# Kernel optimization log

Hardware: AMD Instinct MI355X
Metric: run time of the kernel (lower is better)

The kernel has to match this reference:

```python
import jax, jax.numpy as jnp
import numpy as np

N_E, N_U, N_D = 512, 256, 256
N_A = 16
N_FB = 4
N_SV = 256
N_PV = 64
D_IN0 = 3 * (4 * N_A) + 2 * 4   # 200, fb_block output at layer 0
D_IN = 3 * N_SV + 2 * N_PV      # 896, fb_block output thereafter


def _fb_block(s_v, p_v):
    # s_v: (n_e, d_s); p_v: (n_e, n_e, d_p)
    n_e = N_U + N_D
    su_m = jnp.tile(s_v[:N_U].mean(0)[None, :], (n_e, 1))
    sd_m = jnp.tile(s_v[N_U:].mean(0)[None, :], (n_e, 1))
    pu_m = p_v[:N_U].mean(0)   # (n_e, d_p)
    pd_m = p_v[N_U:].mean(0)
    return jnp.concatenate([su_m, sd_m, pu_m, pd_m, s_v], axis=-1)


def setup_inputs() -> dict:
    key = jax.random.key(0)
    ks = jax.random.split(key, 16)

    def lin(k, fin, fout):
        k1, k2 = jax.random.split(k)
        lim = 1.0 / np.sqrt(fin)
        W = jax.random.uniform(k1, (fin, fout), minval=-lim, maxval=lim, dtype=jnp.float32)
        b = jax.random.uniform(k2, (fout,), minval=-lim, maxval=lim, dtype=jnp.float32)
        return W, b

    V0_W, V0_b = lin(ks[0], D_IN0, N_SV)
    W0_W, W0_b = lin(ks[1], 4, N_PV)
    VrW, Vrb, WrW, Wrb = [], [], [], []
    for i in range(N_FB - 1):
        w, b = lin(ks[2 + i], D_IN, N_SV); VrW.append(w); Vrb.append(b)
        w, b = lin(ks[6 + i], N_PV, N_PV); WrW.append(w); Wrb.append(b)
    Vr_W, Vr_b = jnp.stack(VrW), jnp.stack(Vrb)
    Wr_W, Wr_b = jnp.stack(WrW), jnp.stack(Wrb)
    Vhu_W, Vhu_b = lin(ks[10], D_IN, N_SV)
    Vhd_W, Vhd_b = lin(ks[11], D_IN, N_SV)
    wu_W, wu_b = lin(ks[12], N_SV, N_U)
    wd_W, wd_b = lin(ks[13], N_SV, N_D)
    r = jax.random.normal(ks[14], (N_E, 3), dtype=jnp.float32)
    a = jax.random.normal(ks[15], (N_A, 3), dtype=jnp.float32) * 2.0
    return dict(r=r, a=a, V0_W=V0_W, V0_b=V0_b, Vr_W=Vr_W, Vr_b=Vr_b,
                W0_W=W0_W, W0_b=W0_b, Wr_W=Wr_W, Wr_b=Wr_b,
                Vhu_W=Vhu_W, Vhu_b=Vhu_b, Vhd_W=Vhd_W, Vhd_b=Vhd_b,
                wu_W=wu_W, wu_b=wu_b, wd_W=wd_W, wd_b=wd_b)


def reference(r, a, V0_W, V0_b, Vr_W, Vr_b, W0_W, W0_b, Wr_W, Wr_b,
              Vhu_W, Vhu_b, Vhd_W, Vhd_b, wu_W, wu_b, wd_W, wd_b):
    n_e = N_E
    eye = jnp.eye(n_e, dtype=r.dtype)[:, :, None]
    ra = r[:, None, :] - a[None, :, :]                       # (n_e, n_a, 3)
    ra_len = jnp.linalg.norm(ra, axis=-1, keepdims=True)
    rr = r[None, :, :] - r[:, None, :]                       # (n_e, n_e, 3)
    rr_len = jnp.linalg.norm(rr + eye, axis=-1, keepdims=True)
    s_v = jnp.concatenate([ra, ra_len], axis=-1).reshape(n_e, -1)   # (n_e, 4*n_a)
    p_v = jnp.concatenate([rr, rr_len], axis=-1)                    # (n_e, n_e, 4)
    s_blk = _fb_block(s_v, p_v)
    for l in range(N_FB):
        VW, Vb = (V0_W, V0_b) if l == 0 else (Vr_W[l - 1], Vr_b[l - 1])
        WW, Wb = (W0_W, W0_b) if l == 0 else (Wr_W[l - 1], Wr_b[l - 1])
        s_new = jnp.tanh(s_blk @ VW + Vb)
        s_v = s_new + s_v if s_v.shape[-1] == N_SV else s_new   # residual skips layer 0
        p_new = jnp.tanh(p_v @ WW + Wb)
        p_v = p_new + p_v if p_v.shape[-1] == N_PV else p_new
        s_blk = _fb_block(s_v, p_v)
    s_u = jnp.tanh(s_blk[:N_U] @ Vhu_W + Vhu_b)
    s_d = jnp.tanh(s_blk[N_U:] @ Vhd_W + Vhd_b)
    s_wu = s_u @ wu_W + wu_b                                  # (n_u, n_u)
    s_wd = s_d @ wd_W + wd_b                                  # (n_d, n_d)
    exp_u = jnp.linalg.norm(ra[:N_U], axis=-1, keepdims=True)  # (n_u, n_a, 1)
    exp_d = jnp.linalg.norm(ra[N_U:], axis=-1, keepdims=True)
    orb_u = (s_wu * jnp.exp(-exp_u).sum(axis=1))[None]         # (1, n_u, n_u)
    orb_d = (s_wd * jnp.exp(-exp_d).sum(axis=1))[None]
    # logabssumdet with n_det == 1, matrix dim > 1
    sgn_u, log_u = jnp.linalg.slogdet(orb_u)
    sgn_d, log_d = jnp.linalg.slogdet(orb_d)
    psi = (sgn_u * sgn_d * jnp.exp(log_u + log_d)).sum()
    return jnp.log(jnp.abs(psi))
```

## Files before the change

### kernel.cpp

```cpp
#include <hip/hip_runtime.h>
#include <hip/hip_bf16.h>

#define NE 512

__device__ __align__(16) float g_sv0[NE*64];
__device__ __align__(16) float g_sv[2][NE*256];
__device__ __align__(16) float g_pu4[NE*4];
__device__ __align__(16) float g_pd4[NE*4];
__device__ __align__(16) float g_puL[4*NE*64];
__device__ __align__(16) float g_pdL[4*NE*64];
__device__ __align__(16) float g_su0[64];
__device__ __align__(16) float g_sd0[64];
__device__ __align__(16) float g_su[256];
__device__ __align__(16) float g_sd[256];
__device__ __align__(16) float g_part4[4*16*NE*64];
__device__ __align__(16) float g_f[NE];
__device__ __align__(16) float g_hu[256*256];
__device__ __align__(16) float g_hd[256*256];
__device__ __align__(16) float g_orbu[256*256];
__device__ __align__(16) float g_orbd[256*256];
__device__ float g_logs[2];

__device__ __forceinline__ float tanh_fast(float x) {
  float e = __expf(2.f * x);
  return 1.f - 2.f / (e + 1.f);
}

__global__ __launch_bounds__(256) void k_pgeom(const float* __restrict__ r,
                                               const float* __restrict__ a) {
  int j = blockIdx.x, t = threadIdx.x;
  if (j == 0) {
    for (int h = 0; h < 2; ++h) {
      int e = h*256 + t;
      float rx = r[3*e], ry = r[3*e+1], rz = r[3*e+2];
      float facc = 0.f;
      #pragma unroll
      for (int at = 0; at < 16; ++at) {
        float dx = rx - a[3*at], dy = ry - a[3*at+1], dz = rz - a[3*at+2];
        float len = sqrtf(dx*dx + dy*dy + dz*dz);
        g_sv0[e*64 + 4*at + 0] = dx;
        g_sv0[e*64 + 4*at + 1] = dy;
        g_sv0[e*64 + 4*at + 2] = dz;
        g_sv0[e*64 + 4*at + 3] = len;
        facc += expf(-len);
      }
      g_f[e] = facc;
    }
    __syncthreads();
    if (t < 128) {
      int h = t >> 6, c = t & 63;
      float s = 0.f;
      for (int i = 0; i < 256; ++i) s += g_sv0[(h*256 + i)*64 + c];
      (h ? g_sd0 : g_su0)[c] = s * (1.f/256.f);
    }
    __syncthreads();
  }
  float rjx = r[3*j], rjy = r[3*j+1], rjz = r[3*j+2];
  __shared__ float red[4][4];
  for (int h = 0; h < 2; ++h) {
    int i = h*256 + t;
    float dx = rjx - r[3*i], dy = rjy - r[3*i+1], dz = rjz - r[3*i+2];
    float ee = (i == j) ? 1.f : 0.f;
    float ex = dx+ee, ey = dy+ee, ez = dz+ee;
    float len = sqrtf(ex*ex + ey*ey + ez*ez);
    float v0 = dx, v1 = dy, v2 = dz, v3 = len;
    #pragma unroll
    for (int m = 1; m < 64; m <<= 1) {
      v0 += __shfl_xor(v0, m); v1 += __shfl_xor(v1, m);
      v2 += __shfl_xor(v2, m); v3 += __shfl_xor(v3, m);
    }
    if ((t & 63) == 0) {
      int wv = t >> 6;
      red[wv][0]=v0; red[wv][1]=v1; red[wv][2]=v2; red[wv][3]=v3;
    }
    __syncthreads();
    if (t == 0) {
      float* dst = h ? g_pd4 : g_pu4;
      #pragma unroll
      for (int c = 0; c < 4; ++c)
        dst[j*4 + c] = (red[0][c]+red[1][c]+red[2][c]+red[3][c]) * (1.f/256.f);
    }
    __syncthreads();
  }
}

__global__ __launch_bounds__(256, 4) void k_pchain(const float* __restrict__ W0,
                                                   const float* __restrict__ b0,
                                                   const float* __restrict__ Wr,
                                                   const float* __restrict__ brs,
                                                   const float* __restrict__ r) {
  __shared__ __align__(16) float xbuf[4][32*64];
  int t = threadIdx.x, lane = t & 63, wv = t >> 6;
  int gw = blockIdx.x*4 + wv;
  int j = gw >> 4, chunk = gw & 15;
  int i0 = chunk * 32;
  float* xb = xbuf[wv];
  float rjx = r[3*j], rjy = r[3*j+1], rjz = r[3*j+2];
  float macc0 = 0.f, macc1 = 0.f, macc2 = 0.f, macc3 = 0.f;
  {
    float w0 = W0[lane], w1 = W0[64+lane], w2 = W0[128+lane], w3 = W0[192+lane];
    float bb = b0[lane];
    for (int ii = 0; ii < 32; ++ii) {
      int i = i0 + ii;
      float dx = rjx - r[3*i], dy = rjy - r[3*i+1], dz = rjz - r[3*i+2];
      float ee = (i == j) ? 1.f : 0.f;
      float ex = dx+ee, ey = dy+ee, ez = dz+ee;
      float len = sqrtf(ex*ex + ey*ey + ez*ez);
      float y = tanh_fast(bb + dx*w0 + dy*w1 + dz*w2 + len*w3);
      xb[ii*64 + lane] = y;
      macc0 += y;
    }
  }
  for (int l = 0; l < 3; ++l) {
    const float* W = Wr + l*4096;
    float wcol[64];
    #pragma unroll
    for (int k = 0; k < 64; ++k) wcol[k] = W[k*64 + lane];
    float bb = brs[l*64 + lane];
    float mac = 0.f;
    for (int ii = 0; ii < 32; ++ii) {
      const float* row = &xb[ii*64];
      float x = row[lane];
      float acc = bb;
      #pragma unroll
      for (int g = 0; g < 16; ++g) {
        float4 pv = *(const float4*)&row[4*g];
        acc += pv.x*wcol[4*g] + pv.y*wcol[4*g+1] + pv.z*wcol[4*g+2] + pv.w*wcol[4*g+3];
      }
      float y = tanh_fast(acc) + x;
      xb[ii*64 + lane] = y;
      mac += y;
    }
    if (l == 0) macc1 = mac;
    else if (l == 1) macc2 = mac;
    else macc3 = mac;
  }
  int base = chunk*(NE*64) + j*64 + lane;
  g_part4[0*(16*NE*64) + base] = macc0;
  g_part4[1*(16*NE*64) + base] = macc1;
  g_part4[2*(16*NE*64) + base] = macc2;
  g_part4[3*(16*NE*64) + base] = macc3;
}

__global__ __launch_bounds__(256) void k_reduce_p() {
  int idx = blockIdx.x*256 + threadIdx.x;
  int l = idx >> 16;
  int rem = idx & 65535;
  int half = rem >> 15;
  int r2 = rem & 32767;
  int j = r2 >> 6, c = r2 & 63;
  const float* pp = g_part4 + l*(16*NE*64) + half*(8*NE*64) + j*64 + c;
  float s = 0.f;
  #pragma unroll
  for (int ch = 0; ch < 8; ++ch) s += pp[ch*(NE*64)];
  (half ? g_pdL : g_puL)[l*(NE*64) + j*64 + c] = s * (1.f/256.f);
}

__global__ __launch_bounds__(256) void k_smean(int svsel) {
  int h = blockIdx.x, t = threadIdx.x;
  const float* sv = g_sv[svsel];
  float s = 0.f;
  for (int i = 0; i < 256; ++i) s += sv[(h*256 + i)*256 + t];
  (h ? g_sd : g_su)[t] = s * (1.f/256.f);
}

template<int PUK, int SVK, int MEANK>
__global__ __launch_bounds__(256) void k_smm(int which, const float* __restrict__ W,
                                             const float* __restrict__ Wb,
                                             const float* __restrict__ W2,
                                             const float* __restrict__ Wb2,
                                             int pl) {
  constexpr int MAINK = 2*PUK + SVK;
  __shared__ __align__(16) float wsl[MAINK*32];
  __shared__ float insl[32*(MAINK+1)];
  __shared__ float biasv[32];
  __shared__ float bred[256];
  const float *pu_p=nullptr, *pd_p=nullptr, *sv_p=nullptr, *su_p=nullptr, *sd_p=nullptr;
  const float *res_p=nullptr, *rs_p=nullptr;
  float* out_p = nullptr;
  int t = threadIdx.x;
  int rg = blockIdx.x, cg = blockIdx.y;
  int grp = 0, rgl = rg;
  if (which >= 4) { grp = rg >> 3; rgl = rg & 7; }
  const float* Wsel = (which >= 4 && grp) ? W2 : W;
  const float* Wbsel = (which >= 4 && grp) ? Wb2 : Wb;
  int in_base = 0, dotanh = 1;
  switch (which) {
    case 0: pu_p=g_pu4; pd_p=g_pd4; su_p=g_su0; sd_p=g_sd0; sv_p=g_sv0;
            out_p=g_sv[0]; in_base=rg*32; break;
    case 1: case 2: case 3:
      pu_p=g_puL + pl*(NE*64); pd_p=g_pdL + pl*(NE*64); su_p=g_su; sd_p=g_sd;
      sv_p=g_sv[(which+1)&1]; res_p=sv_p; out_p=g_sv[which&1]; in_base=rg*32; break;
    case 4: pu_p=g_puL + pl*(NE*64); pd_p=g_pdL + pl*(NE*64); su_p=g_su; sd_p=g_sd;
            sv_p=g_sv[1]; out_p = grp ? g_hd : g_hu; in_base = grp*256 + rgl*32; break;
    default: sv_p = grp ? g_hd : g_hu; out_p = grp ? g_orbd : g_orbu;
             rs_p = g_f + grp*256; in_base = rgl*32; dotanh = 0; break;
  }
  int out_base = (which >= 4) ? rgl*32 : rg*32;
  int col0 = cg * 32;
  for (int idx = t; idx < MAINK*32; idx += 256) {
    int c = idx >> 5, cl = idx & 31;
    wsl[idx] = Wsel[(2*MEANK + c)*256 + col0 + cl];
  }
  for (int rr = 0; rr < 32; ++rr) {
    int row = in_base + rr;
    for (int c = t; c < MAINK; c += 256) {
      float v;
      if (c < PUK) v = pu_p[row*PUK + c];
      else if (c < 2*PUK) v = pd_p[row*PUK + (c - PUK)];
      else v = sv_p[row*SVK + (c - 2*PUK)];
      insl[rr*(MAINK+1) + c] = v;
    }
  }
  {
    int pcol = t & 31, ps = t >> 5;
    float bacc = 0.f;
    if (MEANK > 0) {
      for (int c = ps; c < MEANK; c += 8)
        bacc += su_p[c]*Wsel[c*256 + col0 + pcol] + sd_p[c]*Wsel[(MEANK + c)*256 + col0 + pcol];
    }
    bred[ps*32 + pcol] = bacc;
  }
  __syncthreads();
  if (t < 32) {
    float s = Wbsel[col0 + t];
    #pragma unroll
    for (int p8 = 0; p8 < 8; ++p8) s += bred[p8*32 + t];
    biasv[t] = s;
  }
  __syncthreads();
  int c4 = t & 7, rl = t >> 3;
  float a0 = biasv[4*c4], a1 = biasv[4*c4+1], a2 = biasv[4*c4+2], a3 = biasv[4*c4+3];
  const float* inrow = &insl[rl*(MAINK+1)];
  #pragma unroll 4
  for (int c = 0; c < MAINK; ++c) {
    float iv = inrow[c];
    float4 wv = *(const float4*)&wsl[c*32 + 4*c4];
    a0 += iv*wv.x; a1 += iv*wv.y; a2 += iv*wv.z; a3 += iv*wv.w;
  }
  int rowA = out_base + rl;
  int col = col0 + 4*c4;
  if (dotanh) { a0=tanh_fast(a0); a1=tanh_fast(a1); a2=tanh_fast(a2); a3=tanh_fast(a3); }
  if (res_p) {
    float4 rv = *(const float4*)&res_p[rowA*256 + col];
    a0 += rv.x; a1 += rv.y; a2 += rv.z; a3 += rv.w;
  }
  if (rs_p) { float fsc = rs_p[rowA]; a0*=fsc; a1*=fsc; a2*=fsc; a3*=fsc; }
  float4 ov; ov.x=a0; ov.y=a1; ov.z=a2; ov.w=a3;
  *(float4*)&out_p[rowA*256 + col] = ov;
}

#define REP8(M) M(0) M(1) M(2) M(3) M(4) M(5) M(6) M(7)
#define DPPMAX(v, CTRL) { unsigned _o = (unsigned)__builtin_amdgcn_update_dpp(0, (int)(v), CTRL, 0xf, 0xf, true); \
                          (v) = (v) > _o ? (v) : _o; }

__global__ __launch_bounds__(512, 2) void k_lu() {
  __shared__ __align__(16) float colbuf[2][256];
  __shared__ __align__(16) float prowbuf[2][16*20];
  const float* A = (blockIdx.x == 0) ? g_orbu : g_orbd;
  int t = threadIdx.x;
  int tile_c = t >> 5;
  int tile_r = t & 31;
  int lane = t & 63;
  int br = tile_r * 8;
  int pb = tile_c * 20;
  const float4* Ap = (const float4*)(A + br*256 + tile_c*16);
#define DECLROW(R) float4 M##R##_0 = Ap[R*64+0], M##R##_1 = Ap[R*64+1], \
                          M##R##_2 = Ap[R*64+2], M##R##_3 = Ap[R*64+3];
  REP8(DECLROW)
#undef DECLROW
  unsigned um = 0;
  if (tile_c == 0) {
#define INIT0(R) colbuf[0][br+R] = M##R##_0.x;
    REP8(INIT0)
#undef INIT0
  }
  __syncthreads();
  float prod = 1.f;
  int esum = 0;
  float m0=0,m1=0,m2=0,m3=0,m4=0,m5=0,m6=0,m7=0;
  for (int k = 0; k < 256; ++k) {
    const float* cbin = colbuf[k & 1];
    float4 cv = *(const float4*)&cbin[4*lane];
    float4 ca = *(const float4*)&cbin[br];
    float4 cb2 = *(const float4*)&cbin[br+4];
    bool aliveU = (tile_c*16 + 15) >= k;
    if (k > 0 && aliveU) {
      const float* pwp = &prowbuf[(k-1) & 1][pb];
      float4 P0 = *(const float4*)&pwp[0];
      float4 P1 = *(const float4*)&pwp[4];
      float4 P2 = *(const float4*)&pwp[8];
      float4 P3 = *(const float4*)&pwp[12];
#define UPD(R) { float mr = m##R; \
  M##R##_0.x -= mr*P0.x; M##R##_0.y -= mr*P0.y; M##R##_0.z -= mr*P0.z; M##R##_0.w -= mr*P0.w; \
  M##R##_1.x -= mr*P1.x; M##R##_1.y -= mr*P1.y; M##R##_1.z -= mr*P1.z; M##R##_1.w -= mr*P1.w; \
  M##R##_2.x -= mr*P2.x; M##R##_2.y -= mr*P2.y; M##R##_2.z -= mr*P2.z; M##R##_2.w -= mr*P2.w; \
  M##R##_3.x -= mr*P3.x; M##R##_3.y -= mr*P3.y; M##R##_3.z -= mr*P3.z; M##R##_3.w -= mr*P3.w; }
      REP8(UPD)
#undef UPD
    }
    unsigned b0 = (um & 1u) ? 0u : ((__float_as_uint(fabsf(cv.x)) & 0xFFFFFF00u) | (unsigned)(4*lane+0));
    unsigned b1 = (um & 2u) ? 0u : ((__float_as_uint(fabsf(cv.y)) & 0xFFFFFF00u) | (unsigned)(4*lane+1));
    unsigned b2 = (um & 4u) ? 0u : ((__float_as_uint(fabsf(cv.z)) & 0xFFFFFF00u) | (unsigned)(4*lane+2));
    unsigned b3 = (um & 8u) ? 0u : ((__float_as_uint(fabsf(cv.w)) & 0xFFFFFF00u) | (unsigned)(4*lane+3));
    unsigned bb = max(max(b0,b1), max(b2,b3));
    DPPMAX(bb, 0x111) DPPMAX(bb, 0x112) DPPMAX(bb, 0x114) DPPMAX(bb, 0x118)
    DPPMAX(bb, 0x142) DPPMAX(bb, 0x143)
    bb = (unsigned)__builtin_amdgcn_readlane((int)bb, 63);
    int p = (int)(bb & 255u);
    int wl = p >> 2, cc = p & 3;
    unsigned px = (unsigned)__builtin_amdgcn_readlane((int)__float_as_uint(cv.x), wl);
    unsigned py = (unsigned)__builtin_amdgcn_readlane((int)__float_as_uint(cv.y), wl);
    unsigned pz = (unsigned)__builtin_amdgcn_readlane((int)__float_as_uint(cv.z), wl);
    unsigned pw = (unsigned)__builtin_amdgcn_readlane((int)__float_as_uint(cv.w), wl);
    float piv = __uint_as_float(cc==0 ? px : cc==1 ? py : cc==2 ? pz : pw);
    int ee; float mant = frexpf(fabsf(piv), &ee);
    prod *= mant; esum += ee;
    if ((k & 31) == 31) { int e2; prod = frexpf(prod, &e2); esum += e2; }
    if (wl == lane) um |= 1u << cc;
    if (k == 255) break;
    float rp = 1.0f / piv;
    m0 = ca.x*rp; m1 = ca.y*rp; m2 = ca.z*rp; m3 = ca.w*rp;
    m4 = cb2.x*rp; m5 = cb2.y*rp; m6 = cb2.z*rp; m7 = cb2.w*rp;
    bool aliveK = (tile_c*16 + 15) > k;
    if (aliveK && tile_r == (p >> 3)) {
      float* pw_ = &prowbuf[k & 1][pb];
      switch (p & 7) {
#define PUBC(R) case R: *(float4*)&pw_[0] = M##R##_0; *(float4*)&pw_[4] = M##R##_1; \
                        *(float4*)&pw_[8] = M##R##_2; *(float4*)&pw_[12] = M##R##_3; break;
        REP8(PUBC)
#undef PUBC
      }
    }
    int kn = k + 1;
    if (tile_c == (kn >> 4)) {
      float e0,e1,e2b,e3,e4,e5,e6,e7;
      switch (kn & 15) {
#define EXTC(I, G, C) case I: e0=M0_##G.C; e1=M1_##G.C; e2b=M2_##G.C; e3=M3_##G.C; \
                              e4=M4_##G.C; e5=M5_##G.C; e6=M6_##G.C; e7=M7_##G.C; break;
        EXTC(0,0,x) EXTC(1,0,y) EXTC(2,0,z) EXTC(3,0,w)
        EXTC(4,1,x) EXTC(5,1,y) EXTC(6,1,z) EXTC(7,1,w)
        EXTC(8,2,x) EXTC(9,2,y) EXTC(10,2,z) EXTC(11,2,w)
        EXTC(12,3,x) EXTC(13,3,y) EXTC(14,3,z) EXTC(15,3,w)
#undef EXTC
      }
      float sel;
      switch (p & 7) {
        case 0: sel = e0; break; case 1: sel = e1; break;
        case 2: sel = e2b; break; case 3: sel = e3; break;
        case 4: sel = e4; break; case 5: sel = e5; break;
        case 6: sel = e6; break; default: sel = e7; break;
      }
      int srcl = __builtin_amdgcn_readfirstlane((tile_c & 1)*32 + (p >> 3));
      float pv = __uint_as_float((unsigned)__builtin_amdgcn_readlane(
                   (int)__float_as_uint(sel), srcl));
      float4 w0, w1;
      w0.x = e0 - m0*pv; w0.y = e1 - m1*pv; w0.z = e2b - m2*pv; w0.w = e3 - m3*pv;
      w1.x = e4 - m4*pv; w1.y = e5 - m5*pv; w1.z = e6 - m6*pv; w1.w = e7 - m7*pv;
      *(float4*)&colbuf[kn & 1][br] = w0;
      *(float4*)&colbuf[kn & 1][br+4] = w1;
    }
    __syncthreads();
  }
  if (t == 0) g_logs[blockIdx.x] = logf(prod) + (float)esum * 0.69314718055994531f;
}

__global__ void k_final(float* out) { out[0] = g_logs[0] + g_logs[1]; }

extern "C" void kernel_launch(void* const* d_in, const int* in_sizes, int n_in,
                              void* d_out, int out_size, void* d_ws, size_t ws_size,
                              hipStream_t stream) {
  const float* r     = (const float*)d_in[0];
  const float* a     = (const float*)d_in[1];
  const float* V0_W  = (const float*)d_in[2];
  const float* V0_b  = (const float*)d_in[3];
  const float* Vr_W  = (const float*)d_in[4];
  const float* Vr_b  = (const float*)d_in[5];
  const float* W0_W  = (const float*)d_in[6];
  const float* W0_b  = (const float*)d_in[7];
  const float* Wr_W  = (const float*)d_in[8];
  const float* Wr_b  = (const float*)d_in[9];
  const float* Vhu_W = (const float*)d_in[10];
  const float* Vhu_b = (const float*)d_in[11];
  const float* Vhd_W = (const float*)d_in[12];
  const float* Vhd_b = (const float*)d_in[13];
  const float* wu_W  = (const float*)d_in[14];
  const float* wu_b  = (const float*)d_in[15];
  const float* wd_W  = (const float*)d_in[16];
  const float* wd_b  = (const float*)d_in[17];
  float* out = (float*)d_out;

  k_pgeom<<<512, 256, 0, stream>>>(r, a);
  k_pchain<<<2048, 256, 0, stream>>>(W0_W, W0_b, Wr_W, Wr_b, r);
  k_reduce_p<<<1024, 256, 0, stream>>>();

  k_smm<4,64,64><<<dim3(16,8), 256, 0, stream>>>(0, V0_W, V0_b, nullptr, nullptr, 0);
  k_smean<<<2, 256, 0, stream>>>(0);
  k_smm<64,256,256><<<dim3(16,8), 256, 0, stream>>>(1, Vr_W + 0*896*256, Vr_b + 0,
                                                    nullptr, nullptr, 0);
  k_smean<<<2, 256, 0, stream>>>(1);
  k_smm<64,256,256><<<dim3(16,8), 256, 0, stream>>>(2, Vr_W + 1*896*256, Vr_b + 256,
                                                    nullptr, nullptr, 1);
  k_smean<<<2, 256, 0, stream>>>(0);
  k_smm<64,256,256><<<dim3(16,8), 256, 0, stream>>>(3, Vr_W + 2*896*256, Vr_b + 512,
                                                    nullptr, nullptr, 2);
  k_smean<<<2, 256, 0, stream>>>(1);
  k_smm<64,256,256><<<dim3(16,8), 256, 0, stream>>>(4, Vhu_W, Vhu_b, Vhd_W, Vhd_b, 3);
  k_smm<0,256,0><<<dim3(16,8), 256, 0, stream>>>(6, wu_W, wu_b, wd_W, wd_b, 0);
  k_lu<<<2, 512, 0, stream>>>();
  k_final<<<1, 1, 0, stream>>>(out);
}
```

Measured before the change: 650.9 us.

## Pipeline LU pivot search and defer trailing update off the critical path

The blocked LU kernel now computes the pivot search for the next column inside the wave that owns that column, reducing over only 32 rows with DPP, and publishes the pivot index and value through shared scalars. The full rank-1 update of each thread's register tile is deferred by one step: the pivot row and the next column get the previous update applied on the fly, and the bulk update runs after they are published. This is meant to shorten the serial dependency chain per iteration, since every wave no longer redoes a 256-wide argmax reduction and readlane sequence. In exchange the code carries extra per-iteration register state, and pivot selection moves to a partial reduction that needs the 32-row-per-wave layout to stay correct.

```diff
diff --git a/kernel.cpp b/kernel.cpp
--- a/kernel.cpp
+++ b/kernel.cpp
@@ -251,12 +251,12 @@
 }
 
 #define REP8(M) M(0) M(1) M(2) M(3) M(4) M(5) M(6) M(7)
-#define DPPMAX(v, CTRL) { unsigned _o = (unsigned)__builtin_amdgcn_update_dpp(0, (int)(v), CTRL, 0xf, 0xf, true); \
-                          (v) = (v) > _o ? (v) : _o; }
 
 __global__ __launch_bounds__(512, 2) void k_lu() {
   __shared__ __align__(16) float colbuf[2][256];
   __shared__ __align__(16) float prowbuf[2][16*20];
+  __shared__ unsigned scal_p[2];
+  __shared__ float scal_v[2];
   const float* A = (blockIdx.x == 0) ? g_orbu : g_orbd;
   int t = threadIdx.x;
   int tile_c = t >> 5;
@@ -269,99 +269,117 @@
                           M##R##_2 = Ap[R*64+2], M##R##_3 = Ap[R*64+3];
   REP8(DECLROW)
 #undef DECLROW
-  unsigned um = 0;
+  unsigned um8 = 0;
+#define DPAIR(CTRL) { unsigned ko = (unsigned)__builtin_amdgcn_update_dpp(0, (int)key, CTRL, 0xf, 0xf, true); \
+                      unsigned vo = (unsigned)__builtin_amdgcn_update_dpp(0, (int)__float_as_uint(val), CTRL, 0xf, 0xf, true); \
+                      if (ko > key) { key = ko; val = __uint_as_float(vo); } }
+#define CAND(RR) { unsigned kk = (um8 & (1u<<RR)) ? 0u : ((__float_as_uint(fabsf(e##RR)) & 0xFFFFFF00u) | (unsigned)(br + RR)); \
+                   if (kk > key) { key = kk; val = e##RR; } }
   if (tile_c == 0) {
-#define INIT0(R) colbuf[0][br+R] = M##R##_0.x;
-    REP8(INIT0)
-#undef INIT0
+    float e0 = M0_0.x, e1 = M1_0.x, e2 = M2_0.x, e3 = M3_0.x;
+    float e4 = M4_0.x, e5 = M5_0.x, e6 = M6_0.x, e7 = M7_0.x;
+    float4 w0; w0.x=e0; w0.y=e1; w0.z=e2; w0.w=e3;
+    float4 w1; w1.x=e4; w1.y=e5; w1.z=e6; w1.w=e7;
+    *(float4*)&colbuf[0][br] = w0;
+    *(float4*)&colbuf[0][br+4] = w1;
+    unsigned key = 0; float val = 0.f;
+    REP8(CAND)
+    DPAIR(0x111) DPAIR(0x112) DPAIR(0x114) DPAIR(0x118) DPAIR(0x142)
+    if (tile_r == 31) { scal_p[0] = key & 255u; scal_v[0] = val; }
   }
   __syncthreads();
   float prod = 1.f;
   int esum = 0;
-  float m0=0,m1=0,m2=0,m3=0,m4=0,m5=0,m6=0,m7=0;
+  float mp0=0,mp1=0,mp2=0,mp3=0,mp4=0,mp5=0,mp6=0,mp7=0;
   for (int k = 0; k < 256; ++k) {
-    const float* cbin = colbuf[k & 1];
-    float4 cv = *(const float4*)&cbin[4*lane];
-    float4 ca = *(const float4*)&cbin[br];
-    float4 cb2 = *(const float4*)&cbin[br+4];
-    bool aliveU = (tile_c*16 + 15) >= k;
-    if (k > 0 && aliveU) {
-      const float* pwp = &prowbuf[(k-1) & 1][pb];
-      float4 P0 = *(const float4*)&pwp[0];
-      float4 P1 = *(const float4*)&pwp[4];
-      float4 P2 = *(const float4*)&pwp[8];
-      float4 P3 = *(const float4*)&pwp[12];
-#define UPD(R) { float mr = m##R; \
-  M##R##_0.x -= mr*P0.x; M##R##_0.y -= mr*P0.y; M##R##_0.z -= mr*P0.z; M##R##_0.w -= mr*P0.w; \
-  M##R##_1.x -= mr*P1.x; M##R##_1.y -= mr*P1.y; M##R##_1.z -= mr*P1.z; M##R##_1.w -= mr*P1.w; \
-  M##R##_2.x -= mr*P2.x; M##R##_2.y -= mr*P2.y; M##R##_2.z -= mr*P2.z; M##R##_2.w -= mr*P2.w; \
-  M##R##_3.x -= mr*P3.x; M##R##_3.y -= mr*P3.y; M##R##_3.z -= mr*P3.z; M##R##_3.w -= mr*P3.w; }
-      REP8(UPD)
-#undef UPD
-    }
-    unsigned b0 = (um & 1u) ? 0u : ((__float_as_uint(fabsf(cv.x)) & 0xFFFFFF00u) | (unsigned)(4*lane+0));
-    unsigned b1 = (um & 2u) ? 0u : ((__float_as_uint(fabsf(cv.y)) & 0xFFFFFF00u) | (unsigned)(4*lane+1));
-    unsigned b2 = (um & 4u) ? 0u : ((__float_as_uint(fabsf(cv.z)) & 0xFFFFFF00u) | (unsigned)(4*lane+2));
-    unsigned b3 = (um & 8u) ? 0u : ((__float_as_uint(fabsf(cv.w)) & 0xFFFFFF00u) | (unsigned)(4*lane+3));
-    unsigned bb = max(max(b0,b1), max(b2,b3));
-    DPPMAX(bb, 0x111) DPPMAX(bb, 0x112) DPPMAX(bb, 0x114) DPPMAX(bb, 0x118)
-    DPPMAX(bb, 0x142) DPPMAX(bb, 0x143)
-    bb = (unsigned)__builtin_amdgcn_readlane((int)bb, 63);
-    int p = (int)(bb & 255u);
-    int wl = p >> 2, cc = p & 3;
-    unsigned px = (unsigned)__builtin_amdgcn_readlane((int)__float_as_uint(cv.x), wl);
-    unsigned py = (unsigned)__builtin_amdgcn_readlane((int)__float_as_uint(cv.y), wl);
-    unsigned pz = (unsigned)__builtin_amdgcn_readlane((int)__float_as_uint(cv.z), wl);
-    unsigned pw = (unsigned)__builtin_amdgcn_readlane((int)__float_as_uint(cv.w), wl);
-    float piv = __uint_as_float(cc==0 ? px : cc==1 ? py : cc==2 ? pz : pw);
+    int buf = k & 1;
+    unsigned pk = scal_p[buf];
+    float piv = scal_v[buf];
     int ee; float mant = frexpf(fabsf(piv), &ee);
     prod *= mant; esum += ee;
-    if ((k & 31) == 31) { int e2; prod = frexpf(prod, &e2); esum += e2; }
-    if (wl == lane) um |= 1u << cc;
+    if ((k & 31) == 31) { int e2n; prod = frexpf(prod, &e2n); esum += e2n; }
+    if ((int)(pk >> 3) == tile_r) um8 |= 1u << (pk & 7);
     if (k == 255) break;
     float rp = 1.0f / piv;
-    m0 = ca.x*rp; m1 = ca.y*rp; m2 = ca.z*rp; m3 = ca.w*rp;
-    m4 = cb2.x*rp; m5 = cb2.y*rp; m6 = cb2.z*rp; m7 = cb2.w*rp;
-    bool aliveK = (tile_c*16 + 15) > k;
-    if (aliveK && tile_r == (p >> 3)) {
-      float* pw_ = &prowbuf[k & 1][pb];
-      switch (p & 7) {
-#define PUBC(R) case R: *(float4*)&pw_[0] = M##R##_0; *(float4*)&pw_[4] = M##R##_1; \
-                        *(float4*)&pw_[8] = M##R##_2; *(float4*)&pw_[12] = M##R##_3; break;
-        REP8(PUBC)
-#undef PUBC
+    float4 c0 = *(const float4*)&colbuf[buf][br];
+    float4 c1 = *(const float4*)&colbuf[buf][br+4];
+    float m0 = c0.x*rp, m1 = c0.y*rp, m2 = c0.z*rp, m3 = c0.w*rp;
+    float m4 = c1.x*rp, m5 = c1.y*rp, m6 = c1.z*rp, m7 = c1.w*rp;
+    bool alive = (tile_c*16 + 15) >= (k + 1);
+    float4 PR0, PR1, PR2, PR3;
+    PR0.x=PR0.y=PR0.z=PR0.w=0.f; PR1=PR0; PR2=PR0; PR3=PR0;
+    bool havePR = (k > 0) && alive;
+    if (havePR) {
+      const float* pwp = &prowbuf[buf^1][pb];
+      PR0 = *(const float4*)&pwp[0];
+      PR1 = *(const float4*)&pwp[4];
+      PR2 = *(const float4*)&pwp[8];
+      PR3 = *(const float4*)&pwp[12];
+    }
+    float4 P0, P1, P2, P3;
+    P0.x=P0.y=P0.z=P0.w=0.f; P1=P0; P2=P0; P3=P0;
+    if (alive && (int)(pk >> 3) == tile_r) {
+      float mpsel = 0.f;
+      switch (pk & 7) {
+#define PSELR(R) case R: P0=M##R##_0; P1=M##R##_1; P2=M##R##_2; P3=M##R##_3; mpsel=mp##R; break;
+        REP8(PSELR)
+#undef PSELR
       }
+      P0.x -= mpsel*PR0.x; P0.y -= mpsel*PR0.y; P0.z -= mpsel*PR0.z; P0.w -= mpsel*PR0.w;
+      P1.x -= mpsel*PR1.x; P1.y -= mpsel*PR1.y; P1.z -= mpsel*PR1.z; P1.w -= mpsel*PR1.w;
+      P2.x -= mpsel*PR2.x; P2.y -= mpsel*PR2.y; P2.z -= mpsel*PR2.z; P2.w -= mpsel*PR2.w;
+      P3.x -= mpsel*PR3.x; P3.y -= mpsel*PR3.y; P3.z -= mpsel*PR3.z; P3.w -= mpsel*PR3.w;
+      float* pw_ = &prowbuf[buf][pb];
+      *(float4*)&pw_[0]  = P0;
+      *(float4*)&pw_[4]  = P1;
+      *(float4*)&pw_[8]  = P2;
+      *(float4*)&pw_[12] = P3;
     }
     int kn = k + 1;
     if (tile_c == (kn >> 4)) {
-      float e0,e1,e2b,e3,e4,e5,e6,e7;
+      float e0,e1,e2,e3,e4,e5,e6,e7, prsel, Psel;
       switch (kn & 15) {
-#define EXTC(I, G, C) case I: e0=M0_##G.C; e1=M1_##G.C; e2b=M2_##G.C; e3=M3_##G.C; \
-                              e4=M4_##G.C; e5=M5_##G.C; e6=M6_##G.C; e7=M7_##G.C; break;
+#define EXTC(I, G, C) case I: \
+  e0=M0_##G.C; e1=M1_##G.C; e2=M2_##G.C; e3=M3_##G.C; \
+  e4=M4_##G.C; e5=M5_##G.C; e6=M6_##G.C; e7=M7_##G.C; \
+  prsel=PR##G.C; Psel=P##G.C; break;
         EXTC(0,0,x) EXTC(1,0,y) EXTC(2,0,z) EXTC(3,0,w)
         EXTC(4,1,x) EXTC(5,1,y) EXTC(6,1,z) EXTC(7,1,w)
         EXTC(8,2,x) EXTC(9,2,y) EXTC(10,2,z) EXTC(11,2,w)
         EXTC(12,3,x) EXTC(13,3,y) EXTC(14,3,z) EXTC(15,3,w)
 #undef EXTC
+        default: e0=e1=e2=e3=e4=e5=e6=e7=prsel=Psel=0.f; break;
       }
-      float sel;
-      switch (p & 7) {
-        case 0: sel = e0; break; case 1: sel = e1; break;
-        case 2: sel = e2b; break; case 3: sel = e3; break;
-        case 4: sel = e4; break; case 5: sel = e5; break;
-        case 6: sel = e6; break; default: sel = e7; break;
-      }
-      int srcl = __builtin_amdgcn_readfirstlane((tile_c & 1)*32 + (p >> 3));
-      float pv = __uint_as_float((unsigned)__builtin_amdgcn_readlane(
-                   (int)__float_as_uint(sel), srcl));
-      float4 w0, w1;
-      w0.x = e0 - m0*pv; w0.y = e1 - m1*pv; w0.z = e2b - m2*pv; w0.w = e3 - m3*pv;
-      w1.x = e4 - m4*pv; w1.y = e5 - m5*pv; w1.z = e6 - m6*pv; w1.w = e7 - m7*pv;
-      *(float4*)&colbuf[kn & 1][br] = w0;
-      *(float4*)&colbuf[kn & 1][br+4] = w1;
-    }
+      e0 -= mp0*prsel; e1 -= mp1*prsel; e2 -= mp2*prsel; e3 -= mp3*prsel;
+      e4 -= mp4*prsel; e5 -= mp5*prsel; e6 -= mp6*prsel; e7 -= mp7*prsel;
+      int srcl = __builtin_amdgcn_readfirstlane((lane & 32) | (int)(pk >> 3));
+      float pvk = __uint_as_float((unsigned)__builtin_amdgcn_readlane(
+                     (int)__float_as_uint(Psel), srcl));
+      e0 -= m0*pvk; e1 -= m1*pvk; e2 -= m2*pvk; e3 -= m3*pvk;
+      e4 -= m4*pvk; e5 -= m5*pvk; e6 -= m6*pvk; e7 -= m7*pvk;
+      float4 w0; w0.x=e0; w0.y=e1; w0.z=e2; w0.w=e3;
+      float4 w1; w1.x=e4; w1.y=e5; w1.z=e6; w1.w=e7;
+      *(float4*)&colbuf[buf^1][br]   = w0;
+      *(float4*)&colbuf[buf^1][br+4] = w1;
+      unsigned key = 0; float val = 0.f;
+      REP8(CAND)
+      DPAIR(0x111) DPAIR(0x112) DPAIR(0x114) DPAIR(0x118) DPAIR(0x142)
+      if (tile_r == 31) { scal_p[buf^1] = key & 255u; scal_v[buf^1] = val; }
+    }
+    if (havePR) {
+#define UPD(R) { float mr = mp##R; \
+  M##R##_0.x -= mr*PR0.x; M##R##_0.y -= mr*PR0.y; M##R##_0.z -= mr*PR0.z; M##R##_0.w -= mr*PR0.w; \
+  M##R##_1.x -= mr*PR1.x; M##R##_1.y -= mr*PR1.y; M##R##_1.z -= mr*PR1.z; M##R##_1.w -= mr*PR1.w; \
+  M##R##_2.x -= mr*PR2.x; M##R##_2.y -= mr*PR2.y; M##R##_2.z -= mr*PR2.z; M##R##_2.w -= mr*PR2.w; \
+  M##R##_3.x -= mr*PR3.x; M##R##_3.y -= mr*PR3.y; M##R##_3.z -= mr*PR3.z; M##R##_3.w -= mr*PR3.w; }
+      REP8(UPD)
+#undef UPD
+    }
+    mp0=m0; mp1=m1; mp2=m2; mp3=m3; mp4=m4; mp5=m5; mp6=m6; mp7=m7;
     __syncthreads();
   }
+#undef CAND
+#undef DPAIR
   if (t == 0) g_logs[blockIdx.x] = logf(prod) + (float)esum * 0.69314718055994531f;
 }
 
```

Result: slower. 710.1 us (+9.1%).
